# Kernel optimization log

Hardware: AMD Instinct MI355X
Metric: run time of the kernel (lower is better)

Reference implementation:

```python
import jax, jax.numpy as jnp
import numpy as np

BN_EPS = 1e-3

def hard_sigmoid(x):
    # Keras-style hard sigmoid used by LSTMHardSigmoid recurrent gates
    return jnp.clip(0.2 * x + 0.5, 0.0, 1.0)

def lstm_dir(x, w_ih, w_hh, b, reverse):
    # x: [B,S,D]; w_ih: [4H,D]; w_hh: [4H,H]; b: [4H] (b_ih+b_hh combined)
    H = w_hh.shape[1]
    xg = jnp.einsum('bsd,gd->bsg', x, w_ih) + b  # precompute input projection [B,S,4H]
    if reverse:
        xg = xg[:, ::-1]
    def step(carry, xg_t):
        h, c = carry
        g = xg_t + h @ w_hh.T
        i, f, gg, o = jnp.split(g, 4, axis=-1)  # PyTorch gate order i,f,g,o
        i = hard_sigmoid(i); f = hard_sigmoid(f)
        gg = jnp.tanh(gg); o = hard_sigmoid(o)
        c = f * c + i * gg
        h = o * jnp.tanh(c)
        return (h, c), h
    B = x.shape[0]
    h0 = jnp.zeros((B, H), x.dtype)
    _, hs = jax.lax.scan(step, (h0, h0), jnp.swapaxes(xg, 0, 1))
    hs = jnp.swapaxes(hs, 0, 1)  # [B,S,H]
    if reverse:
        hs = hs[:, ::-1]
    return hs

def bilstm(x, wf_ih, wf_hh, bf, wb_ih, wb_hh, bb):
    fwd = lstm_dir(x, wf_ih, wf_hh, bf, False)
    bwd = lstm_dir(x, wb_ih, wb_hh, bb, True)
    return jnp.concatenate([fwd, bwd], axis=-1)

def setup_inputs() -> dict:
    key = jax.random.key(0)
    ks = iter(jax.random.split(key, 64))
    d = {}
    d['x'] = jax.random.randint(next(ks), (64, 512), 0, 149)
    s = 0.08
    d['emb'] = jax.random.normal(next(ks), (149, 288), jnp.float32) * s
    layers = [(288, 288), (576, 144), (288, 96)]
    for l, (din, h) in enumerate(layers):
        for dr in ('f', 'b'):
            d[f'w_ih_{l}{dr}'] = jax.random.normal(next(ks), (4 * h, din), jnp.float32) * s
            d[f'w_hh_{l}{dr}'] = jax.random.normal(next(ks), (4 * h, h), jnp.float32) * s
            d[f'b_{l}{dr}'] = jax.random.normal(next(ks), (4 * h,), jnp.float32) * s
    d['bn_gamma'] = jnp.ones((576,), jnp.float32)
    d['bn_beta'] = jnp.zeros((576,), jnp.float32)
    d['bn_mean'] = jax.random.normal(next(ks), (576,), jnp.float32) * 0.1
    d['bn_var'] = jax.random.uniform(next(ks), (576,), jnp.float32, 0.5, 1.5)
    d['dense_w'] = jax.random.normal(next(ks), (28, 192), jnp.float32) * s
    d['dense_b'] = jnp.zeros((28,), jnp.float32)
    return d

def reference(x, emb,
              w_ih_0f, w_hh_0f, b_0f, w_ih_0b, w_hh_0b, b_0b,
              w_ih_1f, w_hh_1f, b_1f, w_ih_1b, w_hh_1b, b_1b,
              w_ih_2f, w_hh_2f, b_2f, w_ih_2b, w_hh_2b, b_2b,
              bn_gamma, bn_beta, bn_mean, bn_var, dense_w, dense_b):
    h = emb[x]  # [B,S,288]
    h = bilstm(h, w_ih_0f, w_hh_0f, b_0f, w_ih_0b, w_hh_0b, b_0b)  # [B,S,576]
    # BatchNorm1d in eval mode over channel dim
    h = (h - bn_mean) * jax.lax.rsqrt(bn_var + BN_EPS) * bn_gamma + bn_beta
    h = bilstm(h, w_ih_1f, w_hh_1f, b_1f, w_ih_1b, w_hh_1b, b_1b)  # [B,S,288]
    h = bilstm(h, w_ih_2f, w_hh_2f, b_2f, w_ih_2b, w_hh_2b, b_2b)  # [B,S,192]
    logits = jnp.einsum('bsd,od->bso', h, dense_w) + dense_b
    return jax.nn.softmax(logits, axis=-1)
```

## Files before the change

kernel.cpp:

```cpp
#include <hip/hip_runtime.h>
#include <stdint.h>

typedef __attribute__((ext_vector_type(8))) short short8v;
typedef __attribute__((ext_vector_type(4))) short short4v;
typedef __attribute__((ext_vector_type(4))) float float4v;

__device__ __forceinline__ float bf2f(short u) {
  union { unsigned int i; float f; } v;
  v.i = ((unsigned int)(unsigned short)u) << 16;
  return v.f;
}
__device__ __forceinline__ short f2bf(float f) {
  union { float f; unsigned int i; } v; v.f = f;
  unsigned int x = v.i;
  unsigned int r = (x + 0x7fffu + ((x >> 16) & 1u)) >> 16;
  return (short)r;
}
__device__ __forceinline__ float hsigf(float x) {
  return fminf(fmaxf(fmaf(x, 0.2f, 0.5f), 0.0f), 1.0f);
}
__device__ __forceinline__ float tanhf_fast(float x) {
  float e = __expf(2.0f * x);
  return 1.0f - __fdividef(2.0f, e + 1.0f);
}
__device__ __forceinline__ void gload_lds16(const void* g, void* l) {
  __builtin_amdgcn_global_load_lds((const __attribute__((address_space(1))) void*)g,
                                   (__attribute__((address_space(3))) void*)l, 16, 0, 0);
}
__device__ __forceinline__ short8v gload16_cc(const short* p) {
  short8v r;
  asm volatile("global_load_dwordx4 %0, %1, off sc0 sc1" : "=v"(r) : "v"(p));
  return r;
}

__global__ __launch_bounds__(256)
void prep_misc(const float* __restrict__ wih0f, const float* __restrict__ wih0b,
               const float* __restrict__ whh0f, const float* __restrict__ whh0b,
               const float* __restrict__ wih2f, const float* __restrict__ wih2b,
               const float* __restrict__ whh2f, const float* __restrict__ whh2b,
               const float* __restrict__ whh1f, const float* __restrict__ whh1b,
               const float* __restrict__ b0f, const float* __restrict__ b0b,
               const float* __restrict__ b2f, const float* __restrict__ b2b,
               short* __restrict__ WG0, short* __restrict__ WG2,
               short* __restrict__ WHH0, short* __restrict__ WHH1, short* __restrict__ WHH2,
               float* __restrict__ B0, float* __restrict__ B2) {
  int i = blockIdx.x * 256 + threadIdx.x;
  if (i < 663552) { WG0[i] = f2bf(i < 331776 ? wih0f[i] : wih0b[i - 331776]); return; }
  i -= 663552;
  if (i < 221184) { WG2[i] = f2bf(i < 110592 ? wih2f[i] : wih2b[i - 110592]); return; }
  i -= 221184;
  if (i < 663552) { WHH0[i] = f2bf(i < 331776 ? whh0f[i] : whh0b[i - 331776]); return; }
  i -= 663552;
  if (i < 184320) {
    int n = i / 160, k = i - n * 160;
    float v = 0.0f;
    if (k < 144) v = (n < 576) ? whh1f[n * 144 + k] : whh1b[(n - 576) * 144 + k];
    WHH1[i] = f2bf(v); return;
  }
  i -= 184320;
  if (i < 73728) { WHH2[i] = f2bf(i < 36864 ? whh2f[i] : whh2b[i - 36864]); return; }
  i -= 73728;
  if (i < 2304) { B0[i] = (i < 1152) ? b0f[i] : b0b[i - 1152]; return; }
  i -= 2304;
  if (i < 768) { B2[i] = (i < 384) ? b2f[i] : b2b[i - 384]; return; }
}

__global__ __launch_bounds__(64)
void prep_bn(const float* __restrict__ w1f, const float* __restrict__ w1b,
             const float* __restrict__ bf1, const float* __restrict__ bb1,
             const float* __restrict__ gamma, const float* __restrict__ beta,
             const float* __restrict__ mean, const float* __restrict__ var,
             short* __restrict__ WG1, float* __restrict__ B1) {
  int n = blockIdx.x;
  int lane = threadIdx.x;
  const float* wrow = (n < 576) ? (w1f + (long)n * 576) : (w1b + (long)(n - 576) * 576);
  float bsrc = (n < 576) ? bf1[n] : bb1[n - 576];
  float part = 0.0f;
  for (int k = lane; k < 576; k += 64) {
    float sc = gamma[k] * rsqrtf(var[k] + 1e-3f);
    float off = beta[k] - mean[k] * sc;
    float w = wrow[k];
    WG1[(long)n * 576 + k] = f2bf(w * sc);
    part += w * off;
  }
#pragma unroll
  for (int m = 32; m >= 1; m >>= 1) part += __shfl_xor(part, m, 64);
  if (lane == 0) B1[n] = bsrc + part;
}

__global__ __launch_bounds__(256)
void embed_k(const int* __restrict__ x, const float* __restrict__ emb, short* __restrict__ A0) {
  int p0 = blockIdx.x * 16;
  for (int j = threadIdx.x; j < 16 * 72; j += 256) {
    int p = p0 + j / 72;
    int cc = j - (j / 72) * 72;
    int idx = x[p];
    float4v v = *(const float4v*)(emb + (long)idx * 288 + cc * 4);
    short4v s;
    s[0] = f2bf(v[0]); s[1] = f2bf(v[1]); s[2] = f2bf(v[2]); s[3] = f2bf(v[3]);
    *(short4v*)(A0 + (long)p * 288 + cc * 4) = s;
  }
}

__global__ __launch_bounds__(256)
void gemm_xg(const short* __restrict__ A, const short* __restrict__ W,
             const float* __restrict__ bias, short* __restrict__ C,
             int M, int N, int K, int H4, int H) {
  __shared__ short As[128 * 32];
  __shared__ short Bs[128 * 32];
  const int nbn = N >> 7;
  const int bm = blockIdx.x / nbn;
  const int bn = blockIdx.x - bm * nbn;
  const long m0 = (long)bm << 7;
  const int n0 = bn << 7;
  const int tid = threadIdx.x;
  const int lane = tid & 63, wv = tid >> 6;
  const int wr = wv >> 1, wc = wv & 1;
  const int l15 = lane & 15, l4 = lane >> 4;

  float4v acc[4][4];
#pragma unroll
  for (int j = 0; j < 4; ++j) {
    float bvj = bias[n0 + wc * 64 + j * 16 + l15];
#pragma unroll
    for (int i = 0; i < 4; ++i) acc[i][j] = float4v{bvj, bvj, bvj, bvj};
  }

  for (int kt = 0; kt < K; kt += 32) {
#pragma unroll
    for (int c = 0; c < 2; ++c) {
      int ci = wv * 128 + c * 64 + lane;
      int row = ci >> 2, slot = ci & 3;
      int k8 = slot ^ (row & 3);
      gload_lds16(A + (m0 + row) * K + kt + k8 * 8, &As[ci * 8]);
      gload_lds16(W + (long)(n0 + row) * K + kt + k8 * 8, &Bs[ci * 8]);
    }
    __syncthreads();
    short8v af[4], bf[4];
#pragma unroll
    for (int i = 0; i < 4; ++i) {
      int row = wr * 64 + i * 16 + l15;
      af[i] = *(const short8v*)&As[row * 32 + ((l4 ^ (row & 3)) * 8)];
    }
#pragma unroll
    for (int j = 0; j < 4; ++j) {
      int row = wc * 64 + j * 16 + l15;
      bf[j] = *(const short8v*)&Bs[row * 32 + ((l4 ^ (row & 3)) * 8)];
    }
#pragma unroll
    for (int i = 0; i < 4; ++i)
#pragma unroll
      for (int j = 0; j < 4; ++j)
        acc[i][j] = __builtin_amdgcn_mfma_f32_16x16x32_bf16(af[i], bf[j], acc[i][j], 0, 0, 0);
    __syncthreads();
  }

#pragma unroll
  for (int j = 0; j < 4; ++j) {
    int n = n0 + wc * 64 + j * 16 + l15;
    int dir = n / H4;
    int rem = n - dir * H4;
    int q = rem / H;
    int u = rem - q * H;
    long np = (long)dir * H4 + u * 4 + q;
#pragma unroll
    for (int i = 0; i < 4; ++i) {
#pragma unroll
      for (int r = 0; r < 4; ++r) {
        long row = m0 + wr * 64 + i * 16 + l4 * 4 + r;
        C[row * N + np] = f2bf(acc[i][j][r]);
      }
    }
  }
}

template<int H, int NK, int NU>
__global__ __launch_bounds__(256, 1)
void lstm_rec3(const short* __restrict__ xg, int ldxg,
               const short* __restrict__ whh,
               short* __restrict__ out, int ldo,
               int* __restrict__ cnt) {
  constexpr int KPAD = NK * 32;
  const int dir = blockIdx.x & 1;
  const int us = blockIdx.x >> 1;
  const int tid = threadIdx.x;
  const int lane = tid & 63;
  const int mt = tid >> 6;
  const int l15 = lane & 15, l4 = lane >> 4;
  const int target = NU;
  int* cnt_d = cnt + dir * 512;
  const short* whh_d = whh + (long)dir * (4 * H) * KPAD;
  const int xoff = dir * 4 * H;
  const int ooff = dir * H;
  const int u = us * 16 + l15;

  short8v bw[4][NK];
#pragma unroll
  for (int q = 0; q < 4; ++q)
#pragma unroll
    for (int kk = 0; kk < NK; ++kk)
      bw[q][kk] = *(const short8v*)(whh_d + (long)(q * H + u) * KPAD + kk * 32 + l4 * 8);

  float cst[4] = {0.0f, 0.0f, 0.0f, 0.0f};

  for (int t = 0; t < 512; ++t) {
    const int te = dir ? (511 - t) : t;

    short4v x4[4];
#pragma unroll
    for (int r = 0; r < 4; ++r) {
      const long b_ = mt * 16 + l4 * 4 + r;
      x4[r] = *(const short4v*)(xg + (b_ * 512 + te) * ldxg + xoff + u * 4);
    }

    float4v a0 = {0, 0, 0, 0}, a1 = {0, 0, 0, 0}, a2 = {0, 0, 0, 0}, a3 = {0, 0, 0, 0};
    if (t > 0) {
      const int tp = dir ? (te + 1) : (te - 1);
      while (__hip_atomic_load(cnt_d + (t - 1), __ATOMIC_RELAXED, __HIP_MEMORY_SCOPE_AGENT) < target) {}
      __builtin_amdgcn_sched_barrier(0);
      const short* hbase = out + ((long)(mt * 16 + l15) * 512 + tp) * ldo + ooff + l4 * 8;
      short8v a[NK];
#pragma unroll
      for (int kk = 0; kk < NK; ++kk) a[kk] = gload16_cc(hbase + kk * 32);
      asm volatile("s_waitcnt vmcnt(0)" ::: "memory");
      __builtin_amdgcn_sched_barrier(0);
#pragma unroll
      for (int kk = 0; kk < NK; ++kk) {
        a0 = __builtin_amdgcn_mfma_f32_16x16x32_bf16(a[kk], bw[0][kk], a0, 0, 0, 0);
        a1 = __builtin_amdgcn_mfma_f32_16x16x32_bf16(a[kk], bw[1][kk], a1, 0, 0, 0);
        a2 = __builtin_amdgcn_mfma_f32_16x16x32_bf16(a[kk], bw[2][kk], a2, 0, 0, 0);
        a3 = __builtin_amdgcn_mfma_f32_16x16x32_bf16(a[kk], bw[3][kk], a3, 0, 0, 0);
      }
    }

#pragma unroll
    for (int r = 0; r < 4; ++r) {
      const long b_ = mt * 16 + l4 * 4 + r;
      const long orow = (b_ * 512 + te) * ldo;
      float gi_ = a0[r] + bf2f(x4[r][0]);
      float gf_ = a1[r] + bf2f(x4[r][1]);
      float gg_ = a2[r] + bf2f(x4[r][2]);
      float go_ = a3[r] + bf2f(x4[r][3]);
      float iv = hsigf(gi_);
      float fv = hsigf(gf_);
      float gv = tanhf_fast(gg_);
      float ov = hsigf(go_);
      float cn = fv * cst[r] + iv * gv;
      cst[r] = cn;
      float hv = ov * tanhf_fast(cn);
      __hip_atomic_store(out + orow + ooff + u, f2bf(hv),
                         __ATOMIC_RELAXED, __HIP_MEMORY_SCOPE_AGENT);
    }

    asm volatile("s_waitcnt vmcnt(0)" ::: "memory");
    __syncthreads();
    if (tid == 0)
      __hip_atomic_fetch_add(cnt_d + t, 1, __ATOMIC_RELAXED, __HIP_MEMORY_SCOPE_AGENT);
  }
}

__global__ __launch_bounds__(256)
void dense_sm(const short* __restrict__ h, const float* __restrict__ w,
              const float* __restrict__ b, float* __restrict__ out) {
  __shared__ float wl[28 * 192];
  for (int i = threadIdx.x; i < 28 * 192; i += 256) wl[i] = w[i];
  __syncthreads();
  long m = (long)blockIdx.x * 256 + threadIdx.x;
  const short* hr = h + m * 192;
  float acc[28];
#pragma unroll
  for (int o = 0; o < 28; ++o) acc[o] = b[o];
  for (int cch = 0; cch < 24; ++cch) {
    short8v hv = *(const short8v*)(hr + cch * 8);
    float hf[8];
#pragma unroll
    for (int j = 0; j < 8; ++j) hf[j] = bf2f(hv[j]);
#pragma unroll
    for (int o = 0; o < 28; ++o) {
      const float* wp = &wl[o * 192 + cch * 8];
#pragma unroll
      for (int j = 0; j < 8; ++j) acc[o] = fmaf(hf[j], wp[j], acc[o]);
    }
  }
  float mx = acc[0];
#pragma unroll
  for (int o = 1; o < 28; ++o) mx = fmaxf(mx, acc[o]);
  float s = 0.0f;
#pragma unroll
  for (int o = 0; o < 28; ++o) { float e = __expf(acc[o] - mx); acc[o] = e; s += e; }
  float r = __fdividef(1.0f, s);
#pragma unroll
  for (int o = 0; o < 28; ++o) out[m * 28 + o] = acc[o] * r;
}

extern "C" void kernel_launch(void* const* d_in, const int* in_sizes, int n_in,
                              void* d_out, int out_size, void* d_ws, size_t ws_size,
                              hipStream_t stream) {
  const int*   x     = (const int*)d_in[0];
  const float* emb   = (const float*)d_in[1];
  const float* wih0f = (const float*)d_in[2];
  const float* whh0f = (const float*)d_in[3];
  const float* b0f   = (const float*)d_in[4];
  const float* wih0b = (const float*)d_in[5];
  const float* whh0b = (const float*)d_in[6];
  const float* b0b   = (const float*)d_in[7];
  const float* wih1f = (const float*)d_in[8];
  const float* whh1f = (const float*)d_in[9];
  const float* b1f   = (const float*)d_in[10];
  const float* wih1b = (const float*)d_in[11];
  const float* whh1b = (const float*)d_in[12];
  const float* b1b   = (const float*)d_in[13];
  const float* wih2f = (const float*)d_in[14];
  const float* whh2f = (const float*)d_in[15];
  const float* b2f   = (const float*)d_in[16];
  const float* wih2b = (const float*)d_in[17];
  const float* whh2b = (const float*)d_in[18];
  const float* b2b   = (const float*)d_in[19];
  const float* gamma = (const float*)d_in[20];
  const float* beta  = (const float*)d_in[21];
  const float* mean  = (const float*)d_in[22];
  const float* var   = (const float*)d_in[23];
  const float* dw    = (const float*)d_in[24];
  const float* db    = (const float*)d_in[25];

  char* ws = (char*)d_ws;
  size_t off = 0;
  auto alloc = [&](size_t bytes) -> void* {
    void* p = (void*)(ws + off);
    off += (bytes + 255) & ~(size_t)255;
    return p;
  };
  short* A0   = (short*)alloc(32768L * 288 * 2);
  short* XG   = (short*)alloc(32768L * 2304 * 2);
  short* OUT0 = (short*)alloc(32768L * 576 * 2);
  short* OUT1 = (short*)alloc(32768L * 288 * 2);
  short* OUT2 = (short*)alloc(32768L * 192 * 2);
  short* WG0  = (short*)alloc(2304L * 288 * 2);
  short* WG1  = (short*)alloc(1152L * 576 * 2);
  short* WG2  = (short*)alloc(768L * 288 * 2);
  short* WHH0 = (short*)alloc(2304L * 288 * 2);
  short* WHH1 = (short*)alloc(1152L * 160 * 2);
  short* WHH2 = (short*)alloc(768L * 96 * 2);
  float* B0   = (float*)alloc(2304 * 4);
  float* B1   = (float*)alloc(1152 * 4);
  float* B2   = (float*)alloc(768 * 4);
  int* CNT0 = (int*)alloc(2 * 512 * 4);
  int* CNT1 = (int*)alloc(2 * 512 * 4);
  int* CNT2 = (int*)alloc(2 * 512 * 4);
  if (off > ws_size) return;

  hipMemsetAsync(CNT0, 0, 3 * 2 * 512 * 4, stream);

  prep_misc<<<dim3(7068), dim3(256), 0, stream>>>(
      wih0f, wih0b, whh0f, whh0b, wih2f, wih2b, whh2f, whh2b, whh1f, whh1b,
      b0f, b0b, b2f, b2b, WG0, WG2, WHH0, WHH1, WHH2, B0, B2);
  prep_bn<<<dim3(1152), dim3(64), 0, stream>>>(
      wih1f, wih1b, b1f, b1b, gamma, beta, mean, var, WG1, B1);
  embed_k<<<dim3(2048), dim3(256), 0, stream>>>(x, emb, A0);

  gemm_xg<<<dim3(256 * 18), dim3(256), 0, stream>>>(A0, WG0, B0, XG, 32768, 2304, 288, 1152, 288);
  hipLaunchKernelGGL(HIP_KERNEL_NAME(lstm_rec3<288, 9, 18>), dim3(36), dim3(256), 0, stream,
                     XG, 2304, WHH0, OUT0, 576, CNT0);
  gemm_xg<<<dim3(256 * 9), dim3(256), 0, stream>>>(OUT0, WG1, B1, XG, 32768, 1152, 576, 576, 144);
  hipLaunchKernelGGL(HIP_KERNEL_NAME(lstm_rec3<144, 5, 9>), dim3(18), dim3(256), 0, stream,
                     XG, 1152, WHH1, OUT1, 288, CNT1);
  gemm_xg<<<dim3(256 * 6), dim3(256), 0, stream>>>(OUT1, WG2, B2, XG, 32768, 768, 288, 384, 96);
  hipLaunchKernelGGL(HIP_KERNEL_NAME(lstm_rec3<96, 3, 6>), dim3(12), dim3(256), 0, stream,
                     XG, 768, WHH2, OUT2, 192, CNT2);
  dense_sm<<<dim3(128), dim3(256), 0, stream>>>(OUT2, dw, db, (float*)d_out);
}
```

Baseline: 4.217 ms.

## Use per-block flags for layer-0 sync and LDS-local recurrence for layers 1-2

```diff
diff --git a/kernel.cpp b/kernel.cpp
--- a/kernel.cpp
+++ b/kernel.cpp
@@ -32,6 +32,7 @@
   asm volatile("global_load_dwordx4 %0, %1, off sc0 sc1" : "=v"(r) : "v"(p));
   return r;
 }
+__device__ __forceinline__ void pinv(short8v& v) { asm volatile("" : "+v"(v)); }
 
 __global__ __launch_bounds__(256)
 void prep_misc(const float* __restrict__ wih0f, const float* __restrict__ wih0b,
@@ -176,10 +177,10 @@
 
 template<int H, int NK, int NU>
 __global__ __launch_bounds__(256, 1)
-void lstm_rec3(const short* __restrict__ xg, int ldxg,
+void lstm_recX(const short* __restrict__ xg, int ldxg,
                const short* __restrict__ whh,
                short* __restrict__ out, int ldo,
-               int* __restrict__ cnt) {
+               int* __restrict__ fl) {
   constexpr int KPAD = NK * 32;
   const int dir = blockIdx.x & 1;
   const int us = blockIdx.x >> 1;
@@ -187,8 +188,7 @@
   const int lane = tid & 63;
   const int mt = tid >> 6;
   const int l15 = lane & 15, l4 = lane >> 4;
-  const int target = NU;
-  int* cnt_d = cnt + dir * 512;
+  int* fl_d = fl + dir * 512 * 32;
   const short* whh_d = whh + (long)dir * (4 * H) * KPAD;
   const int xoff = dir * 4 * H;
   const int ooff = dir * H;
@@ -198,10 +198,13 @@
 #pragma unroll
   for (int q = 0; q < 4; ++q)
 #pragma unroll
-    for (int kk = 0; kk < NK; ++kk)
+    for (int kk = 0; kk < NK; ++kk) {
       bw[q][kk] = *(const short8v*)(whh_d + (long)(q * H + u) * KPAD + kk * 32 + l4 * 8);
+      pinv(bw[q][kk]);
+    }
 
   float cst[4] = {0.0f, 0.0f, 0.0f, 0.0f};
+  const int flidx = (lane < NU) ? lane : 0;
 
   for (int t = 0; t < 512; ++t) {
     const int te = dir ? (511 - t) : t;
@@ -216,7 +219,8 @@
     float4v a0 = {0, 0, 0, 0}, a1 = {0, 0, 0, 0}, a2 = {0, 0, 0, 0}, a3 = {0, 0, 0, 0};
     if (t > 0) {
       const int tp = dir ? (te + 1) : (te - 1);
-      while (__hip_atomic_load(cnt_d + (t - 1), __ATOMIC_RELAXED, __HIP_MEMORY_SCOPE_AGENT) < target) {}
+      int* fb = fl_d + (t - 1) * 32 + flidx;
+      while (!__all(__hip_atomic_load(fb, __ATOMIC_RELAXED, __HIP_MEMORY_SCOPE_AGENT) != 0)) {}
       __builtin_amdgcn_sched_barrier(0);
       const short* hbase = out + ((long)(mt * 16 + l15) * 512 + tp) * ldo + ooff + l4 * 8;
       short8v a[NK];
@@ -241,21 +245,141 @@
       float gf_ = a1[r] + bf2f(x4[r][1]);
       float gg_ = a2[r] + bf2f(x4[r][2]);
       float go_ = a3[r] + bf2f(x4[r][3]);
-      float iv = hsigf(gi_);
-      float fv = hsigf(gf_);
-      float gv = tanhf_fast(gg_);
-      float ov = hsigf(go_);
+      float iv = hsigf(gi_), fv = hsigf(gf_), gv = tanhf_fast(gg_), ov = hsigf(go_);
       float cn = fv * cst[r] + iv * gv;
       cst[r] = cn;
-      float hv = ov * tanhf_fast(cn);
-      __hip_atomic_store(out + orow + ooff + u, f2bf(hv),
+      __hip_atomic_store(out + orow + ooff + u, f2bf(ov * tanhf_fast(cn)),
                          __ATOMIC_RELAXED, __HIP_MEMORY_SCOPE_AGENT);
     }
 
     asm volatile("s_waitcnt vmcnt(0)" ::: "memory");
     __syncthreads();
     if (tid == 0)
-      __hip_atomic_fetch_add(cnt_d + t, 1, __ATOMIC_RELAXED, __HIP_MEMORY_SCOPE_AGENT);
+      __hip_atomic_store(fl_d + t * 32 + us, 1, __ATOMIC_RELAXED, __HIP_MEMORY_SCOPE_AGENT);
+  }
+}
+
+template<int H, int NK, int NG, int NGW>
+__global__ __launch_bounds__(256, 1)
+void lstm_loc(const short* __restrict__ xg, int ldxg,
+              const short* __restrict__ whh,
+              short* __restrict__ out, int ldo) {
+  constexpr int KPAD = NK * 32;
+  constexpr int HP = KPAD + 8;
+  __shared__ __align__(16) short hbuf[2][16][HP];
+  const int dir = blockIdx.x & 1;
+  const int bg = blockIdx.x >> 1;
+  const int b0 = bg * 16;
+  const int tid = threadIdx.x;
+  const int lane = tid & 63, wv = tid >> 6;
+  const int l15 = lane & 15, l4 = lane >> 4;
+  const short* whh_d = whh + (long)dir * (4 * H) * KPAD;
+  const int xoff = dir * 4 * H;
+  const int ooff = dir * H;
+
+  int u[NGW];
+#pragma unroll
+  for (int j = 0; j < NGW; ++j) {
+    int g = wv + 4 * j; if (g > NG - 1) g = NG - 1;
+    u[j] = g * 16 + l15;
+  }
+
+  {
+    short* hf = &hbuf[0][0][0];
+    for (int i = tid; i < 2 * 16 * HP; i += 256) hf[i] = 0;
+  }
+
+  short8v bw[NGW][4][NK];
+#pragma unroll
+  for (int j = 0; j < NGW; ++j)
+#pragma unroll
+    for (int q = 0; q < 4; ++q)
+#pragma unroll
+      for (int kk = 0; kk < NK; ++kk) {
+        bw[j][q][kk] = *(const short8v*)(whh_d + (long)(q * H + u[j]) * KPAD + kk * 32 + l4 * 8);
+        pinv(bw[j][q][kk]);
+      }
+
+  float cst[NGW][4];
+#pragma unroll
+  for (int j = 0; j < NGW; ++j)
+#pragma unroll
+    for (int r = 0; r < 4; ++r) cst[j][r] = 0.0f;
+
+  const int te0 = dir ? 511 : 0;
+  short4v xc[NGW][4], xn[NGW][4];
+#pragma unroll
+  for (int j = 0; j < NGW; ++j)
+#pragma unroll
+    for (int r = 0; r < 4; ++r)
+      xc[j][r] = *(const short4v*)(xg + ((long)(b0 + l4 * 4 + r) * 512 + te0) * ldxg + xoff + u[j] * 4);
+
+  asm volatile("s_waitcnt lgkmcnt(0)" ::: "memory");
+  __builtin_amdgcn_s_barrier();
+  asm volatile("" ::: "memory");
+
+  for (int t = 0; t < 512; ++t) {
+    const int te = dir ? (511 - t) : t;
+    const int cur = t & 1;
+
+    float4v A[NGW][4];
+#pragma unroll
+    for (int j = 0; j < NGW; ++j)
+#pragma unroll
+      for (int q = 0; q < 4; ++q) A[j][q] = float4v{0, 0, 0, 0};
+
+    if (t > 0) {
+      short8v a[NK];
+#pragma unroll
+      for (int kk = 0; kk < NK; ++kk)
+        a[kk] = *(const short8v*)&hbuf[cur ^ 1][l15][kk * 32 + l4 * 8];
+#pragma unroll
+      for (int j = 0; j < NGW; ++j)
+#pragma unroll
+        for (int kk = 0; kk < NK; ++kk) {
+          A[j][0] = __builtin_amdgcn_mfma_f32_16x16x32_bf16(a[kk], bw[j][0][kk], A[j][0], 0, 0, 0);
+          A[j][1] = __builtin_amdgcn_mfma_f32_16x16x32_bf16(a[kk], bw[j][1][kk], A[j][1], 0, 0, 0);
+          A[j][2] = __builtin_amdgcn_mfma_f32_16x16x32_bf16(a[kk], bw[j][2][kk], A[j][2], 0, 0, 0);
+          A[j][3] = __builtin_amdgcn_mfma_f32_16x16x32_bf16(a[kk], bw[j][3][kk], A[j][3], 0, 0, 0);
+        }
+    }
+
+    if (t < 511) {
+      const int ten = dir ? (te - 1) : (te + 1);
+#pragma unroll
+      for (int j = 0; j < NGW; ++j)
+#pragma unroll
+        for (int r = 0; r < 4; ++r)
+          xn[j][r] = *(const short4v*)(xg + ((long)(b0 + l4 * 4 + r) * 512 + ten) * ldxg + xoff + u[j] * 4);
+    }
+
+#pragma unroll
+    for (int j = 0; j < NGW; ++j)
+#pragma unroll
+      for (int r = 0; r < 4; ++r) {
+        const long b_ = b0 + l4 * 4 + r;
+        const long orow = (b_ * 512 + te) * ldo;
+        float gi_ = A[j][0][r] + bf2f(xc[j][r][0]);
+        float gf_ = A[j][1][r] + bf2f(xc[j][r][1]);
+        float gg_ = A[j][2][r] + bf2f(xc[j][r][2]);
+        float go_ = A[j][3][r] + bf2f(xc[j][r][3]);
+        float iv = hsigf(gi_), fv = hsigf(gf_), gv = tanhf_fast(gg_), ov = hsigf(go_);
+        float cn = fv * cst[j][r] + iv * gv;
+        cst[j][r] = cn;
+        short hb = f2bf(ov * tanhf_fast(cn));
+        hbuf[cur][l4 * 4 + r][u[j]] = hb;
+        out[orow + ooff + u[j]] = hb;
+      }
+
+#pragma unroll
+    for (int j = 0; j < NGW; ++j)
+#pragma unroll
+      for (int r = 0; r < 4; ++r) xc[j][r] = xn[j][r];
+
+    asm volatile("s_waitcnt lgkmcnt(0)" ::: "memory");
+    __builtin_amdgcn_s_barrier();
+    asm volatile("" ::: "memory");
+    __builtin_amdgcn_sched_barrier(0);
   }
 }
 
@@ -344,12 +468,10 @@
   float* B0   = (float*)alloc(2304 * 4);
   float* B1   = (float*)alloc(1152 * 4);
   float* B2   = (float*)alloc(768 * 4);
-  int* CNT0 = (int*)alloc(2 * 512 * 4);
-  int* CNT1 = (int*)alloc(2 * 512 * 4);
-  int* CNT2 = (int*)alloc(2 * 512 * 4);
+  int* FL     = (int*)alloc(2 * 512 * 32 * 4);
   if (off > ws_size) return;
 
-  hipMemsetAsync(CNT0, 0, 3 * 2 * 512 * 4, stream);
+  hipMemsetAsync(FL, 0, 2 * 512 * 32 * 4, stream);
 
   prep_misc<<<dim3(7068), dim3(256), 0, stream>>>(
       wih0f, wih0b, whh0f, whh0b, wih2f, wih2b, whh2f, whh2b, whh1f, whh1b,
@@ -359,13 +481,13 @@
   embed_k<<<dim3(2048), dim3(256), 0, stream>>>(x, emb, A0);
 
   gemm_xg<<<dim3(256 * 18), dim3(256), 0, stream>>>(A0, WG0, B0, XG, 32768, 2304, 288, 1152, 288);
-  hipLaunchKernelGGL(HIP_KERNEL_NAME(lstm_rec3<288, 9, 18>), dim3(36), dim3(256), 0, stream,
-                     XG, 2304, WHH0, OUT0, 576, CNT0);
+  hipLaunchKernelGGL(HIP_KERNEL_NAME(lstm_recX<288, 9, 18>), dim3(36), dim3(256), 0, stream,
+                     XG, 2304, WHH0, OUT0, 576, FL);
   gemm_xg<<<dim3(256 * 9), dim3(256), 0, stream>>>(OUT0, WG1, B1, XG, 32768, 1152, 576, 576, 144);
-  hipLaunchKernelGGL(HIP_KERNEL_NAME(lstm_rec3<144, 5, 9>), dim3(18), dim3(256), 0, stream,
-                     XG, 1152, WHH1, OUT1, 288, CNT1);
+  hipLaunchKernelGGL(HIP_KERNEL_NAME(lstm_loc<144, 5, 9, 3>), dim3(8), dim3(256), 0, stream,
+                     XG, 1152, WHH1, OUT1, 288);
   gemm_xg<<<dim3(256 * 6), dim3(256), 0, stream>>>(OUT1, WG2, B2, XG, 32768, 768, 288, 384, 96);
-  hipLaunchKernelGGL(HIP_KERNEL_NAME(lstm_rec3<96, 3, 6>), dim3(12), dim3(256), 0, stream,
-                     XG, 768, WHH2, OUT2, 192, CNT2);
+  hipLaunchKernelGGL(HIP_KERNEL_NAME(lstm_loc<96, 3, 6, 2>), dim3(8), dim3(256), 0, stream,
+                     XG, 768, WHH2, OUT2, 192);
   dense_sm<<<dim3(128), dim3(256), 0, stream>>>(OUT2, dw, db, (float*)d_out);
 }
```

Result: faster. 3.961 ms (-6.1%).
